# Performance work log

Measured on AMD Instinct MI355X. Metric: run time of the kernel, lower is better.

The kernel has to match this reference:

```python
import jax, jax.numpy as jnp
import numpy as np

B, TOPN, OUT, PAD, IOU_TH, IM = 16, 4, 224, 224, 0.25, 448
HP = IM + 2 * PAD  # padded image side = 896

_ANCHOR_SETTINGS = (
    dict(stride=32, size=48, scale=[2 ** (1. / 3.), 2 ** (2. / 3.)], aspect_ratio=[0.667, 1, 1.5]),
    dict(stride=64, size=96, scale=[2 ** (1. / 3.), 2 ** (2. / 3.)], aspect_ratio=[0.667, 1, 1.5]),
    dict(stride=128, size=192, scale=[1, 2 ** (1. / 3.), 2 ** (2. / 3.)], aspect_ratio=[0.667, 1, 1.5]),
)

def _edge_anchors(input_shape=(IM, IM)):
    # NTS-Net generate_default_anchor_maps: per layer, loop scale then aspect,
    # each emitting an HxW map flattened row-major -> matches tidy conv channel-major flatten.
    out = []
    for a in _ANCHOR_SETTINGS:
        st = a['stride']
        H = int(np.ceil(input_shape[0] / st)); W = int(np.ceil(input_shape[1] / st))
        cy = np.broadcast_to((np.arange(H) * st + st / 2.)[:, None], (H, W))
        cx = np.broadcast_to((np.arange(W) * st + st / 2.)[None, :], (H, W))
        for sc in a['scale']:
            for ar in a['aspect_ratio']:
                h = a['size'] * sc / np.sqrt(ar); w = a['size'] * sc * np.sqrt(ar)
                out.append(np.stack([cy - h / 2., cx - w / 2., cy + h / 2., cx + w / 2.], -1).reshape(-1, 4))
    e = np.concatenate(out, 0)
    return (e + PAD).astype(np.int32)  # module does (edge_anchors + 224).astype(int)


def _conv(x, w, b, stride, pad):
    y = jax.lax.conv_general_dilated(x, w, (stride, stride), [(pad, pad), (pad, pad)],
                                     dimension_numbers=('NCHW', 'OIHW', 'NCHW'))
    return y + b[None, :, None, None]


def _proposal_scores(rpn, w1, b1, w2, b2, w3, b3, wt1, bt1, wt2, bt2, wt3, bt3):
    d1 = jax.nn.relu(_conv(rpn, w1, b1, 1, 1))   # [B,128,14,14]
    d2 = jax.nn.relu(_conv(d1, w2, b2, 2, 1))    # [B,128,7,7]
    d3 = jax.nn.relu(_conv(d2, w3, b3, 2, 1))    # [B,128,4,4]
    bsz = rpn.shape[0]
    t1 = _conv(d1, wt1, bt1, 1, 0).reshape(bsz, -1)  # [B,1176]
    t2 = _conv(d2, wt2, bt2, 1, 0).reshape(bsz, -1)  # [B,294]
    t3 = _conv(d3, wt3, bt3, 1, 0).reshape(bsz, -1)  # [B,144]
    return jnp.concatenate([t1, t2, t3], axis=1)     # [B,1614]


def _nms_topn(scores, boxes, areas):
    # greedy hard NMS, fixed TOPN picks, suppress iou >= IOU_TH (matches upstream hard_nms)
    def step(s, _):
        i = jnp.argmax(s)
        sb = boxes[i]
        iy = jnp.clip(jnp.minimum(boxes[:, 2], sb[2]) - jnp.maximum(boxes[:, 0], sb[0]), 0.)
        ix = jnp.clip(jnp.minimum(boxes[:, 3], sb[3]) - jnp.maximum(boxes[:, 1], sb[1]), 0.)
        inter = iy * ix
        iou = inter / (areas + areas[i] - inter)
        return jnp.where(iou >= IOU_TH, -jnp.inf, s), i
    _, idxs = jax.lax.scan(step, scores, None, length=TOPN)
    return idxs  # [TOPN] int


def _crop_resize(x, anchors, top_idx):
    # batched replacement of the per-(i,j) F.interpolate(x_pad[i,:,y0:y1,x0:x1], 224, bilinear, align_corners=True)
    x_pad = jnp.pad(x, ((0, 0), (0, 0), (PAD, PAD), (PAD, PAD)))
    xp = jnp.transpose(x_pad, (0, 2, 3, 1))            # [B,HP,HP,3]
    bxs = anchors[top_idx].astype(jnp.float32)          # [B,T,4] (y0,x0,y1,x1)
    y0, x0, y1, x1 = bxs[..., 0], bxs[..., 1], bxs[..., 2], bxs[..., 3]
    t = jnp.arange(OUT, dtype=jnp.float32) / (OUT - 1)  # align_corners=True grid
    ys = y0[..., None] + t * (y1 - y0 - 1.)[..., None]  # [B,T,S] src rows in padded img
    xs = x0[..., None] + t * (x1 - x0 - 1.)[..., None]
    yi0 = jnp.floor(ys).astype(jnp.int32); yi1 = jnp.minimum(yi0 + 1, HP - 1)
    xi0 = jnp.floor(xs).astype(jnp.int32); xi1 = jnp.minimum(xi0 + 1, HP - 1)
    wy = (ys - yi0)[..., :, None, None]                 # [B,T,S,1,1]
    wx = (xs - xi0)[..., None, :, None]                 # [B,T,1,S,1]
    b = jnp.arange(x.shape[0])[:, None, None, None]
    g = lambda yi, xi: xp[b, yi[..., :, None], xi[..., None, :]]  # [B,T,S,S,3]
    v = (g(yi0, xi0) * (1 - wy) * (1 - wx) + g(yi0, xi1) * (1 - wy) * wx
         + g(yi1, xi0) * wy * (1 - wx) + g(yi1, xi1) * wy * wx)
    return jnp.transpose(v, (0, 1, 4, 2, 3))            # [B,T,3,S,S]


def setup_inputs() -> dict:
    key = jax.random.key(0)
    ks = jax.random.split(key, 16)
    he = lambda k, shape, fan: jax.random.normal(k, shape, jnp.float32) * np.sqrt(2.0 / fan)
    inp = {
        'x': jax.random.normal(ks[0], (B, 3, IM, IM), jnp.float32),
        'rpn_feature': jax.random.uniform(ks[1], (B, 2048, 14, 14), jnp.float32),
        'w_down1': he(ks[2], (128, 2048, 3, 3), 2048 * 9), 'b_down1': jnp.zeros((128,), jnp.float32),
        'w_down2': he(ks[3], (128, 128, 3, 3), 128 * 9),   'b_down2': jnp.zeros((128,), jnp.float32),
        'w_down3': he(ks[4], (128, 128, 3, 3), 128 * 9),   'b_down3': jnp.zeros((128,), jnp.float32),
        'w_tidy1': he(ks[5], (6, 128, 1, 1), 128),         'b_tidy1': jnp.zeros((6,), jnp.float32),
        'w_tidy2': he(ks[6], (6, 128, 1, 1), 128),         'b_tidy2': jnp.zeros((6,), jnp.float32),
        'w_tidy3': he(ks[7], (9, 128, 1, 1), 128),         'b_tidy3': jnp.zeros((9,), jnp.float32),
        'anchors': jnp.asarray(_edge_anchors(), jnp.int32),  # [1614,4]
    }
    return inp


def reference(x, rpn_feature, w_down1, b_down1, w_down2, b_down2, w_down3, b_down3,
              w_tidy1, b_tidy1, w_tidy2, b_tidy2, w_tidy3, b_tidy3, anchors):
    rpn_score = _proposal_scores(rpn_feature, w_down1, b_down1, w_down2, b_down2, w_down3, b_down3,
                                 w_tidy1, b_tidy1, w_tidy2, b_tidy2, w_tidy3, b_tidy3)
    boxes = anchors.astype(jnp.float32)
    areas = (boxes[:, 2] - boxes[:, 0]) * (boxes[:, 3] - boxes[:, 1])
    top_idx = jax.vmap(lambda s: _nms_topn(s, boxes, areas))(rpn_score)       # [B,TOPN]
    top_prob = jnp.take_along_axis(rpn_score, top_idx, axis=1)                # [B,TOPN]
    part_imgs = _crop_resize(x, anchors, top_idx).reshape(B * TOPN, 3, OUT, OUT)
    return part_imgs, top_idx, top_prob, rpn_score
```

## Files before the change

kernel.cpp:

```cpp
#include <hip/hip_runtime.h>
#include <math.h>

#define BATCH 16
#define TOPN 4
#define OUTS 224
#define PADW 224
#define IM 448
#define HP 896
#define NA 1614
#define IC1 2048
#define C128 128

#define N_PART (BATCH*TOPN*3*OUTS*OUTS)
#define OFF_TOPIDX  (N_PART)
#define OFF_TOPPROB (N_PART + BATCH*TOPN)
#define OFF_SCORE   (N_PART + 2*BATCH*TOPN)

#define WS_D1 0
#define WS_IDX (BATCH*C128*196)
#define WS_WT  (WS_IDX + 64)
#define NWT1 (9*2048*128)
#define NWT2 (9*128*128)
#define NRPNT (BATCH*196*IC1)

typedef __attribute__((ext_vector_type(8))) short frag8;
typedef __attribute__((ext_vector_type(16))) float acc16;
typedef __attribute__((ext_vector_type(4)))  float acc4;

__device__ __forceinline__ unsigned short f2bf(float f) {
    unsigned int u = __float_as_uint(f);
    u = (u + 0x7fffu + ((u >> 16) & 1u)) >> 16;
    return (unsigned short)u;
}
__device__ __forceinline__ float bf2f(unsigned short h) {
    return __uint_as_float(((unsigned int)h) << 16);
}
__device__ __forceinline__ void cvt4(const float* v, ushort4* h, ushort4* lo) {
    unsigned short hh[4], ll[4];
#pragma unroll
    for (int e = 0; e < 4; ++e) { hh[e] = f2bf(v[e]); ll[e] = f2bf(v[e] - bf2f(hh[e])); }
    *h  = make_ushort4(hh[0], hh[1], hh[2], hh[3]);
    *lo = make_ushort4(ll[0], ll[1], ll[2], ll[3]);
}

__device__ __forceinline__ void wrepack_body(const float* __restrict__ w,
                                             unsigned short* __restrict__ w_hi,
                                             unsigned short* __restrict__ w_lo,
                                             int IC, int i) {
    if (i >= 128 * IC) return;
    int oc = i / IC, ic = i % IC;
    const float* src = w + (size_t)(oc * IC + ic) * 9;
#pragma unroll
    for (int tap = 0; tap < 9; ++tap) {
        float v = src[tap];
        unsigned short h = f2bf(v);
        size_t gi = ((size_t)tap * 128 + oc) * IC + ic;
        w_hi[gi] = h;
        w_lo[gi] = f2bf(v - bf2f(h));
    }
}

__device__ __forceinline__ void w1frag_body(const float* __restrict__ w1,
                                            unsigned short* __restrict__ w1h,
                                            unsigned short* __restrict__ w1l,
                                            int i) {
    if (i >= 9 * 32768) return;
    int l  = i & 63;
    int ot = (i >> 6) & 3;
    int c  = (i >> 8) & 3;
    int h  = (i >> 10) & 1;
    int kg = (i >> 11) & 15;
    int t  = i >> 15;
    int oc  = ot * 32 + (l & 31);
    int ic0 = kg * 128 + h * 64 + c * 16 + (l >> 5) * 8;
    const float* src = w1 + ((size_t)oc * IC1 + ic0) * 9 + t;
    frag8 hv, lv;
#pragma unroll
    for (int e = 0; e < 8; ++e) {
        float v = src[e * 9];
        unsigned short hs = f2bf(v);
        hv[e] = (short)hs;
        lv[e] = (short)f2bf(v - bf2f(hs));
    }
    size_t dst = (size_t)i * 8;
    *(frag8*)&w1h[dst] = hv;
    *(frag8*)&w1l[dst] = lv;
}

__global__ __launch_bounds__(256) void k_prep(
    const float* __restrict__ w1, unsigned short* __restrict__ w1h, unsigned short* __restrict__ w1l,
    const float* __restrict__ w2, unsigned short* __restrict__ w2h, unsigned short* __restrict__ w2l,
    const float* __restrict__ w3, unsigned short* __restrict__ w3h, unsigned short* __restrict__ w3l,
    const float* __restrict__ rpn, unsigned short* __restrict__ TH, unsigned short* __restrict__ TL,
    const float* __restrict__ b1, float* __restrict__ d1) {
    __shared__ float tile[64 * 201];
    const int tid = threadIdx.x;
    const int blk = blockIdx.x;
    if (blk < 1152) {
        w1frag_body(w1, w1h, w1l, blk * 256 + tid);
    } else if (blk < 1216) {
        wrepack_body(w2, w2h, w2l, C128, (blk - 1152) * 256 + tid);
    } else if (blk < 1280) {
        wrepack_body(w3, w3h, w3l, C128, (blk - 1216) * 256 + tid);
    } else if (blk < 1792) {
        const int bb = blk - 1280;
        const int b = bb & 15, icg = bb >> 4;
        const int ic0 = icg * 64;
        for (int qq = tid; qq < 3136; qq += 256) {
            int icl = qq / 49, r = qq % 49, p = r * 4;
            const float4 v = *(const float4*)&rpn[(size_t)(b * IC1 + ic0 + icl) * 196 + p];
            tile[icl * 201 + p + 0] = v.x;
            tile[icl * 201 + p + 1] = v.y;
            tile[icl * 201 + p + 2] = v.z;
            tile[icl * 201 + p + 3] = v.w;
        }
        __syncthreads();
        for (int qq = tid; qq < 3136; qq += 256) {
            int px = qq >> 4, ic4 = (qq & 15) * 4;
            float vv[4];
#pragma unroll
            for (int e = 0; e < 4; ++e) vv[e] = tile[(ic4 + e) * 201 + px];
            ushort4 h4, l4; cvt4(vv, &h4, &l4);
            size_t gi = (size_t)(b * 196 + px) * IC1 + ic0 + ic4;
            *(ushort4*)&TH[gi] = h4;
            *(ushort4*)&TL[gi] = l4;
        }
    } else {
        int i = (blk - 1792) * 256 + tid;
        if (i < BATCH * C128 * 196) d1[i] = b1[i & 127];
    }
}

__global__ __launch_bounds__(512, 1) void k_conv1_mfma(const unsigned short* __restrict__ rpnTH,
                                                       const unsigned short* __restrict__ rpnTL,
                                                       const unsigned short* __restrict__ wfh,
                                                       const unsigned short* __restrict__ wfl,
                                                       float* __restrict__ d1) {
    __shared__ unsigned short inH[256 * 72];
    __shared__ unsigned short inL[256 * 72];

    const int tid = threadIdx.x;
    const int b = blockIdx.x >> 4, kg = blockIdx.x & 15;
    const int l = tid & 63, w = tid >> 6;
    const int ln = l & 31, q = l >> 5;
    const int mtw = w & 3, ntw = w >> 2;

    for (int i = tid; i < 256 * 72; i += 512) { inH[i] = 0; inL[i] = 0; }

    acc16 acc[2][2];
#pragma unroll
    for (int mt = 0; mt < 2; ++mt)
#pragma unroll
        for (int nt = 0; nt < 2; ++nt)
#pragma unroll
            for (int r = 0; r < 16; ++r) acc[mt][nt][r] = 0.f;

    int posa[2];
#pragma unroll
    for (int mt = 0; mt < 2; ++mt) {
        int px = (mtw * 2 + mt) * 32 + ln;
        posa[mt] = (px < 196) ? ((px / 14) * 16 + (px % 14)) : 0;
    }

    const size_t wb0 = (size_t)kg * 16384 + (size_t)l * 8;
    __syncthreads();

    for (int half = 0; half < 2; ++half) {
        const int ics = kg * 128 + half * 64;
        for (int qq = tid; qq < 1568; qq += 512) {
            int px = qq >> 3, ic8 = (qq & 7) * 8;
            size_t gi = (size_t)(b * 196 + px) * IC1 + ics + ic8;
            frag8 h8 = *(const frag8*)&rpnTH[gi];
            frag8 l8 = *(const frag8*)&rpnTL[gi];
            int pos = (px / 14 + 1) * 16 + (px % 14 + 1);
            *(frag8*)&inH[pos * 72 + ic8] = h8;
            *(frag8*)&inL[pos * 72 + ic8] = l8;
        }
        __syncthreads();

        const size_t wbh = wb0 + (size_t)half * 8192;
#pragma unroll
        for (int tap = 0; tap < 9; ++tap) {
            const unsigned short* WH = wfh + wbh + (size_t)tap * 262144;
            const unsigned short* WL = wfl + wbh + (size_t)tap * 262144;
            const int off = (tap / 3) * 16 + (tap % 3);
#pragma unroll
            for (int c = 0; c < 4; ++c) {
                frag8 bH[2], bL[2];
#pragma unroll
                for (int nt = 0; nt < 2; ++nt) {
                    const int o2 = c * 2048 + (ntw * 2 + nt) * 512;
                    bH[nt] = *(const frag8*)&WH[o2];
                    bL[nt] = *(const frag8*)&WL[o2];
                }
                const int ko = c * 16 + q * 8;
                frag8 aH[2], aL[2];
#pragma unroll
                for (int mt = 0; mt < 2; ++mt) {
                    int pp = (posa[mt] + off) * 72 + ko;
                    aH[mt] = *(const frag8*)&inH[pp];
                    aL[mt] = *(const frag8*)&inL[pp];
                }
#pragma unroll
                for (int mt = 0; mt < 2; ++mt)
#pragma unroll
                    for (int nt = 0; nt < 2; ++nt) {
                        acc[mt][nt] = __builtin_amdgcn_mfma_f32_32x32x16_bf16(aH[mt], bH[nt], acc[mt][nt], 0, 0, 0);
                        acc[mt][nt] = __builtin_amdgcn_mfma_f32_32x32x16_bf16(aH[mt], bL[nt], acc[mt][nt], 0, 0, 0);
                        acc[mt][nt] = __builtin_amdgcn_mfma_f32_32x32x16_bf16(aL[mt], bH[nt], acc[mt][nt], 0, 0, 0);
                    }
            }
        }
        __syncthreads();
    }

#pragma unroll
    for (int mt = 0; mt < 2; ++mt)
#pragma unroll
        for (int nt = 0; nt < 2; ++nt) {
            int oc = (ntw * 2 + nt) * 32 + ln;
#pragma unroll
            for (int r = 0; r < 16; ++r) {
                int m = (r & 3) + 8 * (r >> 2) + 4 * q;
                int px = (mtw * 2 + mt) * 32 + m;
                if (px < 196)
                    atomicAdd(&d1[(size_t)(b * 196 + px) * 128 + oc], acc[mt][nt][r]);
            }
        }
}

__global__ __launch_bounds__(512, 1) void k_tail(
    const float* __restrict__ d1,
    const unsigned short* __restrict__ w2h, const unsigned short* __restrict__ w2l,
    const unsigned short* __restrict__ w3h, const unsigned short* __restrict__ w3l,
    const float* __restrict__ b2, const float* __restrict__ b3,
    const float* __restrict__ wt1, const float* __restrict__ bt1,
    const float* __restrict__ wt2, const float* __restrict__ bt2,
    const float* __restrict__ wt3, const float* __restrict__ bt3,
    const int* __restrict__ anchors,
    float* __restrict__ score_out, float* __restrict__ out_idx,
    float* __restrict__ out_prob, int* __restrict__ idx_ws) {
    extern __shared__ char smem[];
    unsigned short* inH = (unsigned short*)(smem);
    unsigned short* inL = (unsigned short*)(smem + 43776);
    unsigned short* wHs = (unsigned short*)(smem + 87552);
    unsigned short* wLs = (unsigned short*)(smem + 105984);
    unsigned short* t1H = (unsigned short*)(smem + 124416);
    unsigned short* t1L = (unsigned short*)(smem + 126720);
    float*  d2f  = (float*)(smem + 129024);
    float*  sbuf = (float*)(smem + 154112);
    unsigned short* dhH = (unsigned short*)(smem);
    unsigned short* dhL = (unsigned short*)(smem + 27648);
    float*  d3f  = (float*)(smem + 55296);
    unsigned short* t2H = (unsigned short*)(smem + 63488);
    unsigned short* t2L = (unsigned short*)(smem + 65792);
    unsigned short* w3H = (unsigned short*)(smem + 68096);
    unsigned short* w3L = (unsigned short*)(smem + 86528);
    float* wt3s = (float*)(smem);
    float* y0s = (float*)(smem + 6464);
    float* x0s = (float*)(smem + 12928);
    float* y1s = (float*)(smem + 19392);
    float* x1s = (float*)(smem + 25856);
    float* ars = (float*)(smem + 32320);
    float* rv  = (float*)(smem + 38784);
    int*   ri  = (int*)(smem + 39808);

    const int tid = threadIdx.x;
    const int b = blockIdx.x;
    const int l = tid & 63, w = tid >> 6;
    const int ln = l & 31, q = l >> 5;
    const int l16 = l & 15, q4 = l >> 4;

    for (int i = tid; i < 304 * 72; i += 512) { inH[i] = 0; inL[i] = 0; }

    acc16 c2;
    acc4 t1a[2];
#pragma unroll
    for (int r = 0; r < 16; ++r) c2[r] = 0.f;
#pragma unroll
    for (int i = 0; i < 2; ++i)
#pragma unroll
        for (int r = 0; r < 4; ++r) t1a[i][r] = 0.f;

    const int mtw = w & 1, ntw = w >> 1;
    int posa2;
    {
        int px = mtw * 32 + ln;
        posa2 = (px < 49) ? ((px / 7) * 32 + (px % 7) * 2) : 256;
    }
    __syncthreads();

    for (int half = 0; half < 2; ++half) {
        const int ics = half * 64;
        for (int qq = tid; qq < 3136; qq += 512) {
            int px = qq >> 4, ic4 = (qq & 15) * 4;
            float4 v = *(const float4*)&d1[(size_t)(b * 196 + px) * 128 + ics + ic4];
            float vv[4] = {fmaxf(v.x, 0.f), fmaxf(v.y, 0.f), fmaxf(v.z, 0.f), fmaxf(v.w, 0.f)};
            ushort4 h4, l4; cvt4(vv, &h4, &l4);
            int pos = (px / 14 + 1) * 16 + (px % 14 + 1);
            *(ushort4*)&inH[pos * 72 + ic4] = h4;
            *(ushort4*)&inL[pos * 72 + ic4] = l4;
        }
        for (int qq = tid; qq < 1024; qq += 512) {
            int m = qq >> 6, k = qq & 63;
            float v = (m < 6) ? wt1[m * 128 + ics + k] : 0.f;
            unsigned short h = f2bf(v);
            t1H[m * 72 + k] = h;
            t1L[m * 72 + k] = f2bf(v - bf2f(h));
        }
        ushort4 pwh[4], pwl[4];
#pragma unroll
        for (int it = 0; it < 4; ++it) {
            int qq = tid + it * 512;
            int oc = qq >> 4, ic4 = (qq & 15) * 4;
            size_t gi = ((size_t)(0 * 128 + oc)) * C128 + ics + ic4;
            pwh[it] = *(const ushort4*)&w2h[gi];
            pwl[it] = *(const ushort4*)&w2l[gi];
        }
        __syncthreads();

        for (int tap = 0; tap < 9; ++tap) {
#pragma unroll
            for (int it = 0; it < 4; ++it) {
                int qq = tid + it * 512;
                int oc = qq >> 4, ic4 = (qq & 15) * 4;
                *(ushort4*)&wHs[oc * 72 + ic4] = pwh[it];
                *(ushort4*)&wLs[oc * 72 + ic4] = pwl[it];
            }
            if (tap < 8) {
#pragma unroll
                for (int it = 0; it < 4; ++it) {
                    int qq = tid + it * 512;
                    int oc = qq >> 4, ic4 = (qq & 15) * 4;
                    size_t gi = ((size_t)((tap + 1) * 128 + oc)) * C128 + ics + ic4;
                    pwh[it] = *(const ushort4*)&w2h[gi];
                    pwl[it] = *(const ushort4*)&w2l[gi];
                }
            }
            __syncthreads();
            const int off = (tap / 3) * 16 + (tap % 3);
#pragma unroll
            for (int c = 0; c < 4; ++c) {
                const int ko = c * 16 + q * 8;
                int pp = (posa2 + off) * 72 + ko;
                frag8 aH = *(const frag8*)&inH[pp];
                frag8 aL = *(const frag8*)&inL[pp];
                int oc = ntw * 32 + ln;
                frag8 bH = *(const frag8*)&wHs[oc * 72 + ko];
                frag8 bL = *(const frag8*)&wLs[oc * 72 + ko];
                c2 = __builtin_amdgcn_mfma_f32_32x32x16_bf16(aH, bH, c2, 0, 0, 0);
                c2 = __builtin_amdgcn_mfma_f32_32x32x16_bf16(aH, bL, c2, 0, 0, 0);
                c2 = __builtin_amdgcn_mfma_f32_32x32x16_bf16(aL, bH, c2, 0, 0, 0);
            }
            __syncthreads();
        }

#pragma unroll
        for (int i = 0; i < 2; ++i) {
            int px = (w * 2 + i) * 16 + l16;
            int pos = (px < 196) ? ((px / 14 + 1) * 16 + (px % 14 + 1)) : 256;
#pragma unroll
            for (int c = 0; c < 2; ++c) {
                int ko = c * 32 + q4 * 8;
                frag8 aH = *(const frag8*)&t1H[l16 * 72 + ko];
                frag8 aL = *(const frag8*)&t1L[l16 * 72 + ko];
                frag8 bH = *(const frag8*)&inH[pos * 72 + ko];
                frag8 bL = *(const frag8*)&inL[pos * 72 + ko];
                t1a[i] = __builtin_amdgcn_mfma_f32_16x16x32_bf16(aH, bH, t1a[i], 0, 0, 0);
                t1a[i] = __builtin_amdgcn_mfma_f32_16x16x32_bf16(aH, bL, t1a[i], 0, 0, 0);
                t1a[i] = __builtin_amdgcn_mfma_f32_16x16x32_bf16(aL, bH, t1a[i], 0, 0, 0);
            }
        }
        __syncthreads();
    }

    {
        int oc = ntw * 32 + ln;
        float bias = b2[oc];
#pragma unroll
        for (int r = 0; r < 16; ++r) {
            int m = (r & 3) + 8 * (r >> 2) + 4 * q;
            int px = mtw * 32 + m;
            if (px < 49) d2f[px * 128 + oc] = fmaxf(c2[r] + bias, 0.f);
        }
    }
#pragma unroll
    for (int i = 0; i < 2; ++i) {
        int px = (w * 2 + i) * 16 + l16;
#pragma unroll
        for (int r = 0; r < 4; ++r) {
            int oc = q4 * 4 + r;
            if (oc < 6 && px < 196) {
                float v = t1a[i][r] + bt1[oc];
                sbuf[oc * 196 + px] = v;
                score_out[b * NA + oc * 196 + px] = v;
            }
        }
    }
    __syncthreads();

    for (int i = tid; i < 192 * 72; i += 512) { dhH[i] = 0; dhL[i] = 0; }

    acc16 c3;
    acc4 t2a;
#pragma unroll
    for (int r = 0; r < 16; ++r) c3[r] = 0.f;
#pragma unroll
    for (int r = 0; r < 4; ++r) t2a[r] = 0.f;

    const int posb3 = (ln < 16) ? ((ln / 4) * 32 + (ln % 4) * 2) : 144;
    const int pxt2 = (w - 4) * 16 + l16;
    const int posbt2 = (w >= 4 && pxt2 < 49) ? ((pxt2 / 7 + 1) * 16 + (pxt2 % 7 + 1)) : 144;
    __syncthreads();

    for (int half = 0; half < 2; ++half) {
        const int ics = half * 64;
        for (int qq = tid; qq < 784; qq += 512) {
            int px = qq >> 4, ic4 = (qq & 15) * 4;
            float4 v = *(const float4*)&d2f[px * 128 + ics + ic4];
            float vv[4] = {v.x, v.y, v.z, v.w};
            ushort4 h4, l4; cvt4(vv, &h4, &l4);
            int pos = (px / 7 + 1) * 16 + (px % 7 + 1);
            *(ushort4*)&dhH[pos * 72 + ic4] = h4;
            *(ushort4*)&dhL[pos * 72 + ic4] = l4;
        }
        for (int qq = tid; qq < 1024; qq += 512) {
            int m = qq >> 6, k = qq & 63;
            float v = (m < 6) ? wt2[m * 128 + ics + k] : 0.f;
            unsigned short h = f2bf(v);
            t2H[m * 72 + k] = h;
            t2L[m * 72 + k] = f2bf(v - bf2f(h));
        }
        ushort4 pwh[4], pwl[4];
#pragma unroll
        for (int it = 0; it < 4; ++it) {
            int qq = tid + it * 512;
            int oc = qq >> 4, ic4 = (qq & 15) * 4;
            size_t gi = ((size_t)(0 * 128 + oc)) * C128 + ics + ic4;
            pwh[it] = *(const ushort4*)&w3h[gi];
            pwl[it] = *(const ushort4*)&w3l[gi];
        }
        __syncthreads();

        for (int tap = 0; tap < 9; ++tap) {
#pragma unroll
            for (int it = 0; it < 4; ++it) {
                int qq = tid + it * 512;
                int oc = qq >> 4, ic4 = (qq & 15) * 4;
                *(ushort4*)&w3H[oc * 72 + ic4] = pwh[it];
                *(ushort4*)&w3L[oc * 72 + ic4] = pwl[it];
            }
            if (tap < 8) {
#pragma unroll
                for (int it = 0; it < 4; ++it) {
                    int qq = tid + it * 512;
                    int oc = qq >> 4, ic4 = (qq & 15) * 4;
                    size_t gi = ((size_t)((tap + 1) * 128 + oc)) * C128 + ics + ic4;
                    pwh[it] = *(const ushort4*)&w3h[gi];
                    pwl[it] = *(const ushort4*)&w3l[gi];
                }
            }
            __syncthreads();
            const int off = (tap / 3) * 16 + (tap % 3);
            if (w < 4) {
#pragma unroll
                for (int c = 0; c < 4; ++c) {
                    const int ko = c * 16 + q * 8;
                    int pp = (posb3 + off) * 72 + ko;
                    frag8 aH = *(const frag8*)&dhH[pp];
                    frag8 aL = *(const frag8*)&dhL[pp];
                    int oc = w * 32 + ln;
                    frag8 bH = *(const frag8*)&w3H[oc * 72 + ko];
                    frag8 bL = *(const frag8*)&w3L[oc * 72 + ko];
                    c3 = __builtin_amdgcn_mfma_f32_32x32x16_bf16(aH, bH, c3, 0, 0, 0);
                    c3 = __builtin_amdgcn_mfma_f32_32x32x16_bf16(aH, bL, c3, 0, 0, 0);
                    c3 = __builtin_amdgcn_mfma_f32_32x32x16_bf16(aL, bH, c3, 0, 0, 0);
                }
            } else if (tap == 0) {
#pragma unroll
                for (int c = 0; c < 2; ++c) {
                    int ko = c * 32 + q4 * 8;
                    frag8 aH = *(const frag8*)&t2H[l16 * 72 + ko];
                    frag8 aL = *(const frag8*)&t2L[l16 * 72 + ko];
                    frag8 bH = *(const frag8*)&dhH[posbt2 * 72 + ko];
                    frag8 bL = *(const frag8*)&dhL[posbt2 * 72 + ko];
                    t2a = __builtin_amdgcn_mfma_f32_16x16x32_bf16(aH, bH, t2a, 0, 0, 0);
                    t2a = __builtin_amdgcn_mfma_f32_16x16x32_bf16(aH, bL, t2a, 0, 0, 0);
                    t2a = __builtin_amdgcn_mfma_f32_16x16x32_bf16(aL, bH, t2a, 0, 0, 0);
                }
            }
            __syncthreads();
        }
    }

    if (w < 4) {
        int oc = w * 32 + ln;
        float bias = b3[oc];
#pragma unroll
        for (int r = 0; r < 16; ++r) {
            int px = (r & 3) + 8 * (r >> 2) + 4 * q;
            if (px < 16) d3f[oc * 16 + px] = fmaxf(c3[r] + bias, 0.f);
        }
    } else {
#pragma unroll
        for (int r = 0; r < 4; ++r) {
            int oc = q4 * 4 + r;
            if (oc < 6 && pxt2 < 49) {
                float v = t2a[r] + bt2[oc];
                sbuf[1176 + oc * 49 + pxt2] = v;
                score_out[b * NA + 1176 + oc * 49 + pxt2] = v;
            }
        }
    }
    for (int i = tid; i < 1152; i += 512) wt3s[i] = wt3[i];
    __syncthreads();

    if (tid < 144) {
        int oc = tid >> 4, px = tid & 15;
        float s = bt3[oc];
        for (int ic = 0; ic < 128; ++ic) s += wt3s[oc * 128 + ic] * d3f[ic * 16 + px];
        sbuf[1470 + oc * 16 + px] = s;
        score_out[b * NA + 1470 + oc * 16 + px] = s;
    }
    for (int j = tid; j < NA; j += 512) {
        int4 a = ((const int4*)anchors)[j];
        float a0 = (float)a.x, a1 = (float)a.y, a2 = (float)a.z, a3 = (float)a.w;
        y0s[j] = a0; x0s[j] = a1; y1s[j] = a2; x1s[j] = a3;
        ars[j] = (a2 - a0) * (a3 - a1);
    }
    __syncthreads();

    for (int it = 0; it < TOPN; ++it) {
        float bv = -INFINITY; int bi = NA;
        for (int j = tid; j < NA; j += 512) {
            float v = sbuf[j];
            if (v > bv || (v == bv && j < bi)) { bv = v; bi = j; }
        }
#pragma unroll
        for (int d = 1; d < 64; d <<= 1) {
            float ov = __shfl_xor(bv, d, 64);
            int   oi = __shfl_xor(bi, d, 64);
            if (ov > bv || (ov == bv && oi < bi)) { bv = ov; bi = oi; }
        }
        if (l == 0) { rv[w] = bv; ri[w] = bi; }
        __syncthreads();
        if (tid == 0) {
            float V = rv[0]; int K = ri[0];
#pragma unroll
            for (int j = 1; j < 8; ++j) {
                float ov = rv[j]; int oi = ri[j];
                if (ov > V || (ov == V && oi < K)) { V = ov; K = oi; }
            }
            ri[8] = K;
            out_idx[b * TOPN + it] = (float)K;
            out_prob[b * TOPN + it] = V;
            idx_ws[b * TOPN + it] = K;
        }
        __syncthreads();
        int K = ri[8];
        float ky0 = y0s[K], kx0 = x0s[K], ky1 = y1s[K], kx1 = x1s[K], ka = ars[K];
        for (int j = tid; j < NA; j += 512) {
            float iy = fmaxf(fminf(y1s[j], ky1) - fmaxf(y0s[j], ky0), 0.f);
            float ix = fmaxf(fminf(x1s[j], kx1) - fmaxf(x0s[j], kx0), 0.f);
            float inter = iy * ix;
            float iou = inter / (ars[j] + ka - inter);
            if (iou >= 0.25f) sbuf[j] = -INFINITY;
        }
        __syncthreads();
    }
}

__global__ __launch_bounds__(256) void k_crop(const float* __restrict__ x,
                                              const int* __restrict__ anchors,
                                              const int* __restrict__ idx_ws,
                                              float* __restrict__ out) {
    int blk = blockIdx.x;
    int crop = blk / OUTS;
    int i = blk % OUTS;
    int j = threadIdx.x;
    if (j >= OUTS) return;
    int b = crop >> 2;
    int a = idx_ws[crop];
    int y0 = anchors[a * 4], x0 = anchors[a * 4 + 1];
    int y1 = anchors[a * 4 + 2], x1 = anchors[a * 4 + 3];

    float ti = (float)i / 223.f;
    float ys = (float)y0 + ti * (float)(y1 - y0 - 1);
    int yi0 = (int)ys;
    int yi1 = min(yi0 + 1, HP - 1);
    float wy = ys - (float)yi0;

    float tj = (float)j / 223.f;
    float xs = (float)x0 + tj * (float)(x1 - x0 - 1);
    int xi0 = (int)xs;
    int xi1 = min(xi0 + 1, HP - 1);
    float wx = xs - (float)xi0;

    int ry0 = yi0 - PADW, ry1 = yi1 - PADW, rx0 = xi0 - PADW, rx1 = xi1 - PADW;
    bool vy0 = (ry0 >= 0) && (ry0 < IM), vy1 = (ry1 >= 0) && (ry1 < IM);
    bool vx0 = (rx0 >= 0) && (rx0 < IM), vx1 = (rx1 >= 0) && (rx1 < IM);

    float w00 = (1.f - wy) * (1.f - wx), w01 = (1.f - wy) * wx;
    float w10 = wy * (1.f - wx), w11 = wy * wx;

#pragma unroll
    for (int c = 0; c < 3; ++c) {
        const float* xp = x + (size_t)(b * 3 + c) * IM * IM;
        float g00 = (vy0 && vx0) ? xp[ry0 * IM + rx0] : 0.f;
        float g01 = (vy0 && vx1) ? xp[ry0 * IM + rx1] : 0.f;
        float g10 = (vy1 && vx0) ? xp[ry1 * IM + rx0] : 0.f;
        float g11 = (vy1 && vx1) ? xp[ry1 * IM + rx1] : 0.f;
        out[(size_t)(crop * 3 + c) * OUTS * OUTS + i * OUTS + j] =
            g00 * w00 + g01 * w01 + g10 * w10 + g11 * w11;
    }
}

extern "C" void kernel_launch(void* const* d_in, const int* in_sizes, int n_in,
                              void* d_out, int out_size, void* d_ws, size_t ws_size,
                              hipStream_t stream) {
    (void)in_sizes; (void)n_in; (void)out_size; (void)ws_size;
    const float* x    = (const float*)d_in[0];
    const float* rpn  = (const float*)d_in[1];
    const float* w1   = (const float*)d_in[2];
    const float* b1   = (const float*)d_in[3];
    const float* w2   = (const float*)d_in[4];
    const float* b2   = (const float*)d_in[5];
    const float* w3   = (const float*)d_in[6];
    const float* b3   = (const float*)d_in[7];
    const float* wt1  = (const float*)d_in[8];
    const float* bt1  = (const float*)d_in[9];
    const float* wt2  = (const float*)d_in[10];
    const float* bt2  = (const float*)d_in[11];
    const float* wt3  = (const float*)d_in[12];
    const float* bt3  = (const float*)d_in[13];
    const int*   anc  = (const int*)d_in[14];

    float* out = (float*)d_out;
    float* ws  = (float*)d_ws;
    float* d1  = ws + WS_D1;
    int*   idxw = (int*)(ws + WS_IDX);
    unsigned short* w1h = (unsigned short*)(ws + WS_WT);
    unsigned short* w1l = w1h + NWT1;
    unsigned short* w2h = w1l + NWT1;
    unsigned short* w2l = w2h + NWT2;
    unsigned short* w3h = w2l + NWT2;
    unsigned short* w3l = w3h + NWT2;
    unsigned short* rpnTH = w3l + NWT2;
    unsigned short* rpnTL = rpnTH + NRPNT;

    static const int TAIL_LDS = 160568;
    hipFuncSetAttribute((const void*)k_tail, hipFuncAttributeMaxDynamicSharedMemorySize, TAIL_LDS);

    k_prep<<<3360, 256, 0, stream>>>(w1, w1h, w1l, w2, w2h, w2l, w3, w3h, w3l,
                                     rpn, rpnTH, rpnTL, b1, d1);
    k_conv1_mfma<<<256, 512, 0, stream>>>(rpnTH, rpnTL, w1h, w1l, d1);
    k_tail<<<BATCH, 512, TAIL_LDS, stream>>>(d1, w2h, w2l, w3h, w3l, b2, b3,
                                             wt1, bt1, wt2, bt2, wt3, bt3, anc,
                                             out + OFF_SCORE, out + OFF_TOPIDX,
                                             out + OFF_TOPPROB, idxw);
    k_crop<<<BATCH * TOPN * OUTS, 256, 0, stream>>>(x, anc, idxw, out);
}
```

Baseline: 291.7 us.

## Split conv1 input-channel halves across blocks with swizzled LDS and prefetched weights

After: 291.9 us. No clear change (+0.0%).

```diff
diff --git a/kernel.cpp b/kernel.cpp
--- a/kernel.cpp
+++ b/kernel.cpp
@@ -131,102 +131,112 @@
     }
 }
 
-__global__ __launch_bounds__(512, 1) void k_conv1_mfma(const unsigned short* __restrict__ rpnTH,
+
+#define LOADB(it, BH0, BH1, BL0, BL1) { \
+    const int o_ = ((it) >> 2) * 262144 + ((it) & 3) * 2048; \
+    BH0 = *(const frag8*)&WHb[o_];       BL0 = *(const frag8*)&WLb[o_]; \
+    BH1 = *(const frag8*)&WHb[o_ + 512]; BL1 = *(const frag8*)&WLb[o_ + 512]; }
+
+#define DOMFMA(it, BH0, BH1, BL0, BL1) { \
+    const int tap_ = (it) >> 2; \
+    const int off_ = (tap_ / 3) * 16 + (tap_ % 3); \
+    const int kb_ = ((it) & 3) * 32 + q * 16; \
+    const int p0_ = posa0 + off_, p1_ = posa1 + off_; \
+    const int by0_ = (p0_ * 128 + kb_) ^ ((p0_ & 7) << 4); \
+    const int by1_ = (p1_ * 128 + kb_) ^ ((p1_ & 7) << 4); \
+    frag8 aH0 = *(const frag8*)((const char*)inH + by0_); \
+    frag8 aL0 = *(const frag8*)((const char*)inL + by0_); \
+    frag8 aH1 = *(const frag8*)((const char*)inH + by1_); \
+    frag8 aL1 = *(const frag8*)((const char*)inL + by1_); \
+    acc00 = __builtin_amdgcn_mfma_f32_32x32x16_bf16(aH0, BH0, acc00, 0, 0, 0); \
+    acc00 = __builtin_amdgcn_mfma_f32_32x32x16_bf16(aH0, BL0, acc00, 0, 0, 0); \
+    acc00 = __builtin_amdgcn_mfma_f32_32x32x16_bf16(aL0, BH0, acc00, 0, 0, 0); \
+    acc01 = __builtin_amdgcn_mfma_f32_32x32x16_bf16(aH0, BH1, acc01, 0, 0, 0); \
+    acc01 = __builtin_amdgcn_mfma_f32_32x32x16_bf16(aH0, BL1, acc01, 0, 0, 0); \
+    acc01 = __builtin_amdgcn_mfma_f32_32x32x16_bf16(aL0, BH1, acc01, 0, 0, 0); \
+    acc10 = __builtin_amdgcn_mfma_f32_32x32x16_bf16(aH1, BH0, acc10, 0, 0, 0); \
+    acc10 = __builtin_amdgcn_mfma_f32_32x32x16_bf16(aH1, BL0, acc10, 0, 0, 0); \
+    acc10 = __builtin_amdgcn_mfma_f32_32x32x16_bf16(aL1, BH0, acc10, 0, 0, 0); \
+    acc11 = __builtin_amdgcn_mfma_f32_32x32x16_bf16(aH1, BH1, acc11, 0, 0, 0); \
+    acc11 = __builtin_amdgcn_mfma_f32_32x32x16_bf16(aH1, BL1, acc11, 0, 0, 0); \
+    acc11 = __builtin_amdgcn_mfma_f32_32x32x16_bf16(aL1, BH1, acc11, 0, 0, 0); }
+
+__global__ __launch_bounds__(512, 4) void k_conv1_mfma(const unsigned short* __restrict__ rpnTH,
                                                        const unsigned short* __restrict__ rpnTL,
                                                        const unsigned short* __restrict__ wfh,
                                                        const unsigned short* __restrict__ wfl,
                                                        float* __restrict__ d1) {
-    __shared__ unsigned short inH[256 * 72];
-    __shared__ unsigned short inL[256 * 72];
+    __shared__ unsigned short inH[256 * 64];
+    __shared__ unsigned short inL[256 * 64];
 
     const int tid = threadIdx.x;
-    const int b = blockIdx.x >> 4, kg = blockIdx.x & 15;
+    const int blk = blockIdx.x;
+    const int b = blk >> 5, s = blk & 31;
+    const int kg = s >> 1, half = s & 1;
     const int l = tid & 63, w = tid >> 6;
     const int ln = l & 31, q = l >> 5;
     const int mtw = w & 3, ntw = w >> 2;
 
-    for (int i = tid; i < 256 * 72; i += 512) { inH[i] = 0; inL[i] = 0; }
-
-    acc16 acc[2][2];
-#pragma unroll
-    for (int mt = 0; mt < 2; ++mt)
-#pragma unroll
-        for (int nt = 0; nt < 2; ++nt)
-#pragma unroll
-            for (int r = 0; r < 16; ++r) acc[mt][nt][r] = 0.f;
-
-    int posa[2];
-#pragma unroll
-    for (int mt = 0; mt < 2; ++mt) {
-        int px = (mtw * 2 + mt) * 32 + ln;
-        posa[mt] = (px < 196) ? ((px / 14) * 16 + (px % 14)) : 0;
-    }
-
-    const size_t wb0 = (size_t)kg * 16384 + (size_t)l * 8;
+    for (int i = tid; i < 2048; i += 512) {
+        ((uint4*)inH)[i] = make_uint4(0u, 0u, 0u, 0u);
+        ((uint4*)inL)[i] = make_uint4(0u, 0u, 0u, 0u);
+    }
+
+    acc16 acc00, acc01, acc10, acc11;
+#pragma unroll
+    for (int r = 0; r < 16; ++r) { acc00[r] = 0.f; acc01[r] = 0.f; acc10[r] = 0.f; acc11[r] = 0.f; }
+
+    const int px0 = mtw * 64 + ln;
+    const int px1 = mtw * 64 + 32 + ln;
+    const int posa0 = (px0 < 196) ? ((px0 / 14) * 16 + (px0 % 14)) : 0;
+    const int posa1 = (px1 < 196) ? ((px1 / 14) * 16 + (px1 % 14)) : 0;
+
+    const unsigned short* WHb = wfh + (size_t)kg * 16384 + half * 8192 + ntw * 1024 + (size_t)l * 8;
+    const unsigned short* WLb = wfl + (size_t)kg * 16384 + half * 8192 + ntw * 1024 + (size_t)l * 8;
+
+    const int ics = kg * 128 + half * 64;
     __syncthreads();
 
-    for (int half = 0; half < 2; ++half) {
-        const int ics = kg * 128 + half * 64;
-        for (int qq = tid; qq < 1568; qq += 512) {
-            int px = qq >> 3, ic8 = (qq & 7) * 8;
-            size_t gi = (size_t)(b * 196 + px) * IC1 + ics + ic8;
-            frag8 h8 = *(const frag8*)&rpnTH[gi];
-            frag8 l8 = *(const frag8*)&rpnTL[gi];
-            int pos = (px / 14 + 1) * 16 + (px % 14 + 1);
-            *(frag8*)&inH[pos * 72 + ic8] = h8;
-            *(frag8*)&inL[pos * 72 + ic8] = l8;
-        }
-        __syncthreads();
-
-        const size_t wbh = wb0 + (size_t)half * 8192;
-#pragma unroll
-        for (int tap = 0; tap < 9; ++tap) {
-            const unsigned short* WH = wfh + wbh + (size_t)tap * 262144;
-            const unsigned short* WL = wfl + wbh + (size_t)tap * 262144;
-            const int off = (tap / 3) * 16 + (tap % 3);
-#pragma unroll
-            for (int c = 0; c < 4; ++c) {
-                frag8 bH[2], bL[2];
-#pragma unroll
-                for (int nt = 0; nt < 2; ++nt) {
-                    const int o2 = c * 2048 + (ntw * 2 + nt) * 512;
-                    bH[nt] = *(const frag8*)&WH[o2];
-                    bL[nt] = *(const frag8*)&WL[o2];
-                }
-                const int ko = c * 16 + q * 8;
-                frag8 aH[2], aL[2];
-#pragma unroll
-                for (int mt = 0; mt < 2; ++mt) {
-                    int pp = (posa[mt] + off) * 72 + ko;
-                    aH[mt] = *(const frag8*)&inH[pp];
-                    aL[mt] = *(const frag8*)&inL[pp];
-                }
-#pragma unroll
-                for (int mt = 0; mt < 2; ++mt)
-#pragma unroll
-                    for (int nt = 0; nt < 2; ++nt) {
-                        acc[mt][nt] = __builtin_amdgcn_mfma_f32_32x32x16_bf16(aH[mt], bH[nt], acc[mt][nt], 0, 0, 0);
-                        acc[mt][nt] = __builtin_amdgcn_mfma_f32_32x32x16_bf16(aH[mt], bL[nt], acc[mt][nt], 0, 0, 0);
-                        acc[mt][nt] = __builtin_amdgcn_mfma_f32_32x32x16_bf16(aL[mt], bH[nt], acc[mt][nt], 0, 0, 0);
-                    }
-            }
-        }
-        __syncthreads();
-    }
-
-#pragma unroll
-    for (int mt = 0; mt < 2; ++mt)
-#pragma unroll
-        for (int nt = 0; nt < 2; ++nt) {
-            int oc = (ntw * 2 + nt) * 32 + ln;
-#pragma unroll
-            for (int r = 0; r < 16; ++r) {
-                int m = (r & 3) + 8 * (r >> 2) + 4 * q;
-                int px = (mtw * 2 + mt) * 32 + m;
-                if (px < 196)
-                    atomicAdd(&d1[(size_t)(b * 196 + px) * 128 + oc], acc[mt][nt][r]);
-            }
-        }
+    for (int qq = tid; qq < 1568; qq += 512) {
+        int px = qq >> 3, ic8 = qq & 7;
+        size_t gi = (size_t)(b * 196 + px) * IC1 + ics + ic8 * 8;
+        frag8 h8 = *(const frag8*)&rpnTH[gi];
+        frag8 l8 = *(const frag8*)&rpnTL[gi];
+        int pos = (px / 14 + 1) * 16 + (px % 14 + 1);
+        int byo = (pos * 128 + ic8 * 16) ^ ((pos & 7) << 4);
+        *(frag8*)((char*)inH + byo) = h8;
+        *(frag8*)((char*)inL + byo) = l8;
+    }
+    __syncthreads();
+
+    frag8 b0H0, b0H1, b0L0, b0L1, b1H0, b1H1, b1L0, b1L1;
+    LOADB(0, b0H0, b0H1, b0L0, b0L1);
+#pragma unroll
+    for (int i2 = 0; i2 < 18; ++i2) {
+        LOADB(i2 * 2 + 1, b1H0, b1H1, b1L0, b1L1);
+        DOMFMA(i2 * 2, b0H0, b0H1, b0L0, b0L1);
+        if (i2 < 17) LOADB(i2 * 2 + 2, b0H0, b0H1, b0L0, b0L1);
+        DOMFMA(i2 * 2 + 1, b1H0, b1H1, b1L0, b1L1);
+    }
+
+    {
+        const int oc0 = ntw * 64 + ln;
+        const int oc1 = ntw * 64 + 32 + ln;
+#pragma unroll
+        for (int r = 0; r < 16; ++r) {
+            int m = (r & 3) + 8 * (r >> 2) + 4 * q;
+            int pxa = mtw * 64 + m;
+            int pxb = mtw * 64 + 32 + m;
+            if (pxa < 196) {
+                atomicAdd(&d1[(size_t)(b * 196 + pxa) * 128 + oc0], acc00[r]);
+                atomicAdd(&d1[(size_t)(b * 196 + pxa) * 128 + oc1], acc01[r]);
+            }
+            if (pxb < 196) {
+                atomicAdd(&d1[(size_t)(b * 196 + pxb) * 128 + oc0], acc10[r]);
+                atomicAdd(&d1[(size_t)(b * 196 + pxb) * 128 + oc1], acc11[r]);
+            }
+        }
+    }
 }
 
 __global__ __launch_bounds__(512, 1) void k_tail(
@@ -653,7 +663,7 @@
 
     k_prep<<<3360, 256, 0, stream>>>(w1, w1h, w1l, w2, w2h, w2l, w3, w3h, w3l,
                                      rpn, rpnTH, rpnTL, b1, d1);
-    k_conv1_mfma<<<256, 512, 0, stream>>>(rpnTH, rpnTL, w1h, w1l, d1);
+    k_conv1_mfma<<<512, 512, 0, stream>>>(rpnTH, rpnTL, w1h, w1l, d1);
     k_tail<<<BATCH, 512, TAIL_LDS, stream>>>(d1, w2h, w2l, w3h, w3l, b2, b3,
                                              wt1, bt1, wt2, bt2, wt3, bt3, anc,
                                              out + OFF_SCORE, out + OFF_TOPIDX,
```

## Restructure conv1 MFMA: pre-padded swizzled bf16 images, finer split-K, drop low-part activations

Applied to the files above, without the earlier changes.

Result: faster. 273.9 us (-6.1%).

```diff
diff --git a/kernel.cpp b/kernel.cpp
--- a/kernel.cpp
+++ b/kernel.cpp
@@ -21,7 +21,7 @@
 #define WS_WT  (WS_IDX + 64)
 #define NWT1 (9*2048*128)
 #define NWT2 (9*128*128)
-#define NRPNT (BATCH*196*IC1)
+#define NIMG (16*32*16384)
 
 typedef __attribute__((ext_vector_type(8))) short frag8;
 typedef __attribute__((ext_vector_type(16))) float acc16;
@@ -64,48 +64,54 @@
                                             unsigned short* __restrict__ w1h,
                                             unsigned short* __restrict__ w1l,
                                             int i) {
-    if (i >= 9 * 32768) return;
-    int l  = i & 63;
-    int ot = (i >> 6) & 3;
-    int c  = (i >> 8) & 3;
-    int h  = (i >> 10) & 1;
-    int kg = (i >> 11) & 15;
-    int t  = i >> 15;
-    int oc  = ot * 32 + (l & 31);
-    int ic0 = kg * 128 + h * 64 + c * 16 + (l >> 5) * 8;
-    const float* src = w1 + ((size_t)oc * IC1 + ic0) * 9 + t;
-    frag8 hv, lv;
-#pragma unroll
-    for (int e = 0; e < 8; ++e) {
-        float v = src[e * 9];
-        unsigned short hs = f2bf(v);
-        hv[e] = (short)hs;
-        lv[e] = (short)f2bf(v - bf2f(hs));
-    }
-    size_t dst = (size_t)i * 8;
-    *(frag8*)&w1h[dst] = hv;
-    *(frag8*)&w1l[dst] = lv;
+    if (i >= 32768) return;
+    int oc5 = i & 31;
+    int q8  = (i >> 5) & 1;
+    int ot  = (i >> 6) & 3;
+    int c   = (i >> 8) & 3;
+    int h   = (i >> 10) & 1;
+    int kg  = (i >> 11) & 15;
+    int oc  = ot * 32 + oc5;
+    int ic0 = kg * 128 + h * 64 + c * 16 + q8 * 8;
+    int l   = q8 * 32 + oc5;
+    const float* src = w1 + ((size_t)oc * IC1 + ic0) * 9;
+    size_t dbase = (size_t)kg * 16384 + h * 8192 + c * 2048 + ot * 512 + l * 8;
+#pragma unroll
+    for (int t = 0; t < 9; ++t) {
+        frag8 hv, lv;
+#pragma unroll
+        for (int e = 0; e < 8; ++e) {
+            float v = src[e * 9 + t];
+            unsigned short hs = f2bf(v);
+            hv[e] = (short)hs;
+            lv[e] = (short)f2bf(v - bf2f(hs));
+        }
+        size_t dst = dbase + (size_t)t * 262144;
+        *(frag8*)&w1h[dst] = hv;
+        *(frag8*)&w1l[dst] = lv;
+    }
 }
 
 __global__ __launch_bounds__(256) void k_prep(
     const float* __restrict__ w1, unsigned short* __restrict__ w1h, unsigned short* __restrict__ w1l,
     const float* __restrict__ w2, unsigned short* __restrict__ w2h, unsigned short* __restrict__ w2l,
     const float* __restrict__ w3, unsigned short* __restrict__ w3h, unsigned short* __restrict__ w3l,
-    const float* __restrict__ rpn, unsigned short* __restrict__ TH, unsigned short* __restrict__ TL,
+    const float* __restrict__ rpn, unsigned short* __restrict__ imgH,
     const float* __restrict__ b1, float* __restrict__ d1) {
     __shared__ float tile[64 * 201];
     const int tid = threadIdx.x;
     const int blk = blockIdx.x;
-    if (blk < 1152) {
+    if (blk < 128) {
         w1frag_body(w1, w1h, w1l, blk * 256 + tid);
-    } else if (blk < 1216) {
-        wrepack_body(w2, w2h, w2l, C128, (blk - 1152) * 256 + tid);
-    } else if (blk < 1280) {
-        wrepack_body(w3, w3h, w3l, C128, (blk - 1216) * 256 + tid);
-    } else if (blk < 1792) {
-        const int bb = blk - 1280;
+    } else if (blk < 192) {
+        wrepack_body(w2, w2h, w2l, C128, (blk - 128) * 256 + tid);
+    } else if (blk < 256) {
+        wrepack_body(w3, w3h, w3l, C128, (blk - 192) * 256 + tid);
+    } else if (blk < 768) {
+        const int bb = blk - 256;
         const int b = bb & 15, icg = bb >> 4;
         const int ic0 = icg * 64;
+        char* img = (char*)(imgH + (size_t)bb * 16384);
         for (int qq = tid; qq < 3136; qq += 256) {
             int icl = qq / 49, r = qq % 49, p = r * 4;
             const float4 v = *(const float4*)&rpn[(size_t)(b * IC1 + ic0 + icl) * 196 + p];
@@ -118,115 +124,119 @@
         for (int qq = tid; qq < 3136; qq += 256) {
             int px = qq >> 4, ic4 = (qq & 15) * 4;
             float vv[4];
-#pragma unroll
-            for (int e = 0; e < 4; ++e) vv[e] = tile[(ic4 + e) * 201 + px];
-            ushort4 h4, l4; cvt4(vv, &h4, &l4);
-            size_t gi = (size_t)(b * 196 + px) * IC1 + ic0 + ic4;
-            *(ushort4*)&TH[gi] = h4;
-            *(ushort4*)&TL[gi] = l4;
+            unsigned short hh[4];
+#pragma unroll
+            for (int e = 0; e < 4; ++e) { vv[e] = tile[(ic4 + e) * 201 + px]; hh[e] = f2bf(vv[e]); }
+            int pos = (px / 14 + 1) * 16 + (px % 14 + 1);
+            int byo = (pos * 128 + ic4 * 2) ^ ((pos & 7) << 4);
+            *(ushort4*)(img + byo) = make_ushort4(hh[0], hh[1], hh[2], hh[3]);
+        }
+        for (int qq = tid; qq < 960; qq += 256) {
+            int hp = qq >> 4, sub = qq & 15;
+            int pos;
+            if (hp < 16)      pos = hp;
+            else if (hp < 32) pos = 240 + (hp - 16);
+            else if (hp < 46) pos = (hp - 31) * 16;
+            else              pos = (hp - 45) * 16 + 15;
+            *(ushort4*)(img + pos * 128 + sub * 8) = make_ushort4(0, 0, 0, 0);
         }
     } else {
-        int i = (blk - 1792) * 256 + tid;
-        if (i < BATCH * C128 * 196) d1[i] = b1[i & 127];
-    }
-}
-
-__global__ __launch_bounds__(512, 1) void k_conv1_mfma(const unsigned short* __restrict__ rpnTH,
-                                                       const unsigned short* __restrict__ rpnTL,
+        int i = (blk - 768) * 256 + tid;
+        int base = i * 4;
+        float4 v;
+        v.x = b1[(base + 0) & 127]; v.y = b1[(base + 1) & 127];
+        v.z = b1[(base + 2) & 127]; v.w = b1[(base + 3) & 127];
+        *(float4*)&d1[base] = v;
+    }
+}
+
+
+#define LOADB(it, BH, BL) { \
+    const int o_ = ((it) >> 2) * 262144 + ((it) & 3) * 2048; \
+    BH = *(const frag8*)&WHb[o_]; BL = *(const frag8*)&WLb[o_]; }
+
+#define DOMFMA(it, BH, BL) { \
+    const int tap_ = (it) >> 2; \
+    const int off_ = (tap_ / 3) * 16 + (tap_ % 3); \
+    const int kb_ = ((it) & 3) * 32 + q * 16; \
+    frag8 aH[4]; \
+    _Pragma("unroll") \
+    for (int mt_ = 0; mt_ < 4; ++mt_) { \
+        const int p_ = posa[mt_] + off_; \
+        const int by_ = (p_ * 128 + kb_) ^ ((p_ & 7) << 4); \
+        aH[mt_] = *(const frag8*)((const char*)inH + by_); \
+    } \
+    _Pragma("unroll") \
+    for (int mt_ = 0; mt_ < 4; ++mt_) { \
+        acc[mt_] = __builtin_amdgcn_mfma_f32_32x32x16_bf16(aH[mt_], BH, acc[mt_], 0, 0, 0); \
+        acc[mt_] = __builtin_amdgcn_mfma_f32_32x32x16_bf16(aH[mt_], BL, acc[mt_], 0, 0, 0); \
+    } }
+
+__global__ __launch_bounds__(512, 4) void k_conv1_mfma(const unsigned short* __restrict__ imgH,
                                                        const unsigned short* __restrict__ wfh,
                                                        const unsigned short* __restrict__ wfl,
                                                        float* __restrict__ d1) {
-    __shared__ unsigned short inH[256 * 72];
-    __shared__ unsigned short inL[256 * 72];
+    __shared__ unsigned short inH[256 * 64];
 
     const int tid = threadIdx.x;
-    const int b = blockIdx.x >> 4, kg = blockIdx.x & 15;
+    const int blk = blockIdx.x;
+    const int b = blk >> 5;
+    const int icg = blk & 31;
     const int l = tid & 63, w = tid >> 6;
     const int ln = l & 31, q = l >> 5;
-    const int mtw = w & 3, ntw = w >> 2;
-
-    for (int i = tid; i < 256 * 72; i += 512) { inH[i] = 0; inL[i] = 0; }
-
-    acc16 acc[2][2];
-#pragma unroll
-    for (int mt = 0; mt < 2; ++mt)
-#pragma unroll
-        for (int nt = 0; nt < 2; ++nt)
-#pragma unroll
-            for (int r = 0; r < 16; ++r) acc[mt][nt][r] = 0.f;
-
-    int posa[2];
-#pragma unroll
-    for (int mt = 0; mt < 2; ++mt) {
-        int px = (mtw * 2 + mt) * 32 + ln;
+    const int mtw = w & 1, ntw = w >> 1;
+
+    {
+        const char* src = (const char*)(imgH + ((size_t)(icg * 16 + b)) * 16384);
+        char* dst = (char*)inH;
+#pragma unroll
+        for (int k = 0; k < 4; ++k) {
+            frag8 v = *(const frag8*)(src + tid * 16 + k * 8192);
+            *(frag8*)(dst + tid * 16 + k * 8192) = v;
+        }
+    }
+
+    acc16 acc[4];
+#pragma unroll
+    for (int mt = 0; mt < 4; ++mt)
+#pragma unroll
+        for (int r = 0; r < 16; ++r) acc[mt][r] = 0.f;
+
+    int posa[4];
+#pragma unroll
+    for (int mt = 0; mt < 4; ++mt) {
+        int px = mtw * 128 + mt * 32 + ln;
         posa[mt] = (px < 196) ? ((px / 14) * 16 + (px % 14)) : 0;
     }
 
-    const size_t wb0 = (size_t)kg * 16384 + (size_t)l * 8;
+    const unsigned short* WHb = wfh + (size_t)icg * 8192 + ntw * 512 + (size_t)l * 8;
+    const unsigned short* WLb = wfl + (size_t)icg * 8192 + ntw * 512 + (size_t)l * 8;
+
     __syncthreads();
 
-    for (int half = 0; half < 2; ++half) {
-        const int ics = kg * 128 + half * 64;
-        for (int qq = tid; qq < 1568; qq += 512) {
-            int px = qq >> 3, ic8 = (qq & 7) * 8;
-            size_t gi = (size_t)(b * 196 + px) * IC1 + ics + ic8;
-            frag8 h8 = *(const frag8*)&rpnTH[gi];
-            frag8 l8 = *(const frag8*)&rpnTL[gi];
-            int pos = (px / 14 + 1) * 16 + (px % 14 + 1);
-            *(frag8*)&inH[pos * 72 + ic8] = h8;
-            *(frag8*)&inL[pos * 72 + ic8] = l8;
-        }
-        __syncthreads();
-
-        const size_t wbh = wb0 + (size_t)half * 8192;
-#pragma unroll
-        for (int tap = 0; tap < 9; ++tap) {
-            const unsigned short* WH = wfh + wbh + (size_t)tap * 262144;
-            const unsigned short* WL = wfl + wbh + (size_t)tap * 262144;
-            const int off = (tap / 3) * 16 + (tap % 3);
-#pragma unroll
-            for (int c = 0; c < 4; ++c) {
-                frag8 bH[2], bL[2];
-#pragma unroll
-                for (int nt = 0; nt < 2; ++nt) {
-                    const int o2 = c * 2048 + (ntw * 2 + nt) * 512;
-                    bH[nt] = *(const frag8*)&WH[o2];
-                    bL[nt] = *(const frag8*)&WL[o2];
-                }
-                const int ko = c * 16 + q * 8;
-                frag8 aH[2], aL[2];
-#pragma unroll
-                for (int mt = 0; mt < 2; ++mt) {
-                    int pp = (posa[mt] + off) * 72 + ko;
-                    aH[mt] = *(const frag8*)&inH[pp];
-                    aL[mt] = *(const frag8*)&inL[pp];
-                }
-#pragma unroll
-                for (int mt = 0; mt < 2; ++mt)
-#pragma unroll
-                    for (int nt = 0; nt < 2; ++nt) {
-                        acc[mt][nt] = __builtin_amdgcn_mfma_f32_32x32x16_bf16(aH[mt], bH[nt], acc[mt][nt], 0, 0, 0);
-                        acc[mt][nt] = __builtin_amdgcn_mfma_f32_32x32x16_bf16(aH[mt], bL[nt], acc[mt][nt], 0, 0, 0);
-                        acc[mt][nt] = __builtin_amdgcn_mfma_f32_32x32x16_bf16(aL[mt], bH[nt], acc[mt][nt], 0, 0, 0);
-                    }
-            }
-        }
-        __syncthreads();
-    }
-
-#pragma unroll
-    for (int mt = 0; mt < 2; ++mt)
-#pragma unroll
-        for (int nt = 0; nt < 2; ++nt) {
-            int oc = (ntw * 2 + nt) * 32 + ln;
+    frag8 b0H, b0L, b1H, b1L;
+    LOADB(0, b0H, b0L);
+#pragma unroll
+    for (int i2 = 0; i2 < 18; ++i2) {
+        LOADB(i2 * 2 + 1, b1H, b1L);
+        DOMFMA(i2 * 2, b0H, b0L);
+        if (i2 < 17) LOADB(i2 * 2 + 2, b0H, b0L);
+        DOMFMA(i2 * 2 + 1, b1H, b1L);
+    }
+
+    {
+        const int oc = ntw * 32 + ln;
+#pragma unroll
+        for (int mt = 0; mt < 4; ++mt) {
 #pragma unroll
             for (int r = 0; r < 16; ++r) {
                 int m = (r & 3) + 8 * (r >> 2) + 4 * q;
-                int px = (mtw * 2 + mt) * 32 + m;
+                int px = mtw * 128 + mt * 32 + m;
                 if (px < 196)
-                    atomicAdd(&d1[(size_t)(b * 196 + px) * 128 + oc], acc[mt][nt][r]);
-            }
-        }
+                    atomicAdd(&d1[(size_t)(b * 196 + px) * 128 + oc], acc[mt][r]);
+            }
+        }
+    }
 }
 
 __global__ __launch_bounds__(512, 1) void k_tail(
@@ -645,15 +655,14 @@
     unsigned short* w2l = w2h + NWT2;
     unsigned short* w3h = w2l + NWT2;
     unsigned short* w3l = w3h + NWT2;
-    unsigned short* rpnTH = w3l + NWT2;
-    unsigned short* rpnTL = rpnTH + NRPNT;
+    unsigned short* imgH = w3l + NWT2;
 
     static const int TAIL_LDS = 160568;
     hipFuncSetAttribute((const void*)k_tail, hipFuncAttributeMaxDynamicSharedMemorySize, TAIL_LDS);
 
-    k_prep<<<3360, 256, 0, stream>>>(w1, w1h, w1l, w2, w2h, w2l, w3, w3h, w3l,
-                                     rpn, rpnTH, rpnTL, b1, d1);
-    k_conv1_mfma<<<256, 512, 0, stream>>>(rpnTH, rpnTL, w1h, w1l, d1);
+    k_prep<<<1160, 256, 0, stream>>>(w1, w1h, w1l, w2, w2h, w2l, w3, w3h, w3l,
+                                     rpn, imgH, b1, d1);
+    k_conv1_mfma<<<512, 512, 0, stream>>>(imgH, w1h, w1l, d1);
     k_tail<<<BATCH, 512, TAIL_LDS, stream>>>(d1, w2h, w2l, w3h, w3l, b2, b3,
                                              wt1, bt1, wt2, bt2, wt3, bt3, anc,
                                              out + OFF_SCORE, out + OFF_TOPIDX,
```
